# Kernel optimization log

Measured on AMD Instinct MI355X. Metric: run time of the kernel, lower is better.

## Reference

```python
import jax, jax.numpy as jnp
import numpy as np

T, B, I, H, E = 32, 128, 64, 128, 4
N_TRAP = 100  # trapezoid intervals -> 101 sample points


def setup_inputs() -> dict:
    key = jax.random.key(0)
    ks = jax.random.split(key, 14)
    s_cell = 1.0 / np.sqrt(I + H)
    s_wh = 1.0 / np.sqrt((I + H) * E)

    def u(k, shape, s):
        return jax.random.uniform(k, shape, jnp.float32, -s, s)

    return {
        "x_time": jax.random.normal(ks[0], (T, B, I), jnp.float32),
        "dt_time": jax.random.uniform(ks[1], (T, B), jnp.float32, 0.01, 1.0),
        "Wh_w": u(ks[2], ((I + H) * E, H * E), s_wh),
        "Wh_b": u(ks[3], (H * E,), s_wh),
        "Wi_w": u(ks[4], (E, I + H, H), s_cell),
        "Wi_b": u(ks[5], (E, H), s_cell),
        "Wf_w": u(ks[6], (E, I + H, H), s_cell),
        "Wf_b": u(ks[7], (E, H), s_cell),
        "Wd_w": u(ks[8], (E, I + H, H), s_cell),
        "Wd_b": u(ks[9], (E, H), s_cell),
        "Wg_w": u(ks[10], (E, I + H, H), s_cell),
        "Wg_b": u(ks[11], (E, H), s_cell),
        "Wo_w": u(ks[12], (E, I + H, H), s_cell),
        "Wo_b": u(ks[13], (E, H), s_cell),
        "alpha": jnp.ones((E, H), jnp.float32) / H,
    }


def reference(x_time, dt_time, Wh_w, Wh_b, Wi_w, Wi_b, Wf_w, Wf_b,
              Wd_w, Wd_b, Wg_w, Wg_b, Wo_w, Wo_b, alpha):
    t_total, batch, in_dim = x_time.shape
    e_types, hid = alpha.shape
    ts_unit = jnp.linspace(0.0, 1.0, N_TRAP + 1, dtype=x_time.dtype)  # [101]

    def step(carry, inp):
        h, c = carry            # each [E,B,H]
        x, dt = inp             # [B,I], [B]
        # hidden_sum = Wh(cat_m([x, h_m]))
        cat = jnp.concatenate(
            [jnp.concatenate([x, h[m]], axis=-1) for m in range(e_types)], axis=-1)  # [B,(I+H)*E]
        hs = (cat @ Wh_w + Wh_b).reshape(batch, e_types, hid).transpose(1, 0, 2)     # [E,B,H]
        iv = jnp.concatenate(
            [jnp.broadcast_to(x[None], (e_types, batch, in_dim)), hs], axis=-1)       # [E,B,I+H]

        def gate(W, b):
            return jnp.einsum('ebd,edh->ebh', iv, W) + b[:, None, :]

        i_g = jax.nn.sigmoid(gate(Wi_w, Wi_b))
        f_g = jax.nn.sigmoid(gate(Wf_w, Wf_b))
        g = f_g * c + i_g * jnp.tanh(gate(Wg_w, Wg_b))   # curr_g
        delta = jnp.exp(gate(Wd_w, Wd_b))                 # curr_delta
        o = jax.nn.sigmoid(gate(Wo_w, Wo_b))              # curr_o
        diff = c - g                                      # prev_c - curr_g

        c_new = g + diff * jnp.exp(-delta * dt[None, :, None])  # c_t at dt
        h_new = o * jnp.tanh(c_new)
        lam = jnp.einsum('eh,ebh->eb', alpha, h_new)             # intensity at dt

        # trapezoidal integration of intensity over [0, dt], 100 intervals
        ts = dt[:, None] * ts_unit                                # [B,101]
        cv = g[:, :, None, :] + diff[:, :, None, :] * jnp.exp(
            -delta[:, :, None, :] * ts[None, :, :, None])         # [E,B,101,H]
        fv = jnp.einsum('eh,ebth->ebt', alpha, o[:, :, None, :] * jnp.tanh(cv))  # [E,B,101]
        integ = (dt[None, :] / N_TRAP) * (
            jnp.sum(fv, axis=-1) - 0.5 * (fv[..., 0] + fv[..., -1]))  # [E,B]

        return (h_new, c_new), (lam.T, integ.T)  # outputs [B,E]

    h0 = jnp.zeros((e_types, batch, hid), x_time.dtype)
    c0 = jnp.zeros_like(h0)
    _, (lambdas, lambda_integrals) = jax.lax.scan(step, (h0, c0), (x_time, dt_time))
    return lambdas, lambda_integrals  # each [T,B,E]
```

## Files before the change

### kernel.cpp

```cpp
#include <hip/hip_runtime.h>

#define OFF_WALL   0
#define OFF_BIAS   196608
#define OFF_WHHH   199680
#define OFF_WGH    330752
#define OFF_XG     494592
#define OFF_HBUF   21466112

typedef _Float16 half2_t __attribute__((ext_vector_type(2)));

__device__ __forceinline__ float fast_sig(float x) {
    return __fdividef(1.f, 1.f + __expf(-x));
}
__device__ __forceinline__ float sig_e(float y) {
    return __builtin_amdgcn_rcpf(__expf(y) + 1.f);
}
__device__ __forceinline__ unsigned pack2h(float a, float b) {
    _Float16 ha = (_Float16)a, hb = (_Float16)b;
    unsigned short ua = __builtin_bit_cast(unsigned short, ha);
    unsigned short ub = __builtin_bit_cast(unsigned short, hb);
    return ((unsigned)ub << 16) | ua;
}
__device__ __forceinline__ float dot2(unsigned w, unsigned h, float acc) {
    return __builtin_amdgcn_fdot2(__builtin_bit_cast(half2_t, w),
                                  __builtin_bit_cast(half2_t, h), acc, false);
}

__global__ __launch_bounds__(256) void k0_pack(
    const float* __restrict__ Wh_w, const float* __restrict__ Wh_b,
    const float* __restrict__ Wi_w, const float* __restrict__ Wi_b,
    const float* __restrict__ Wf_w, const float* __restrict__ Wf_b,
    const float* __restrict__ Wd_w, const float* __restrict__ Wd_b,
    const float* __restrict__ Wg_w, const float* __restrict__ Wg_b,
    const float* __restrict__ Wo_w, const float* __restrict__ Wo_b,
    float* __restrict__ ws)
{
    const float* gw[5] = {Wi_w, Wf_w, Wd_w, Wg_w, Wo_w};
    const float* gb[5] = {Wi_b, Wf_b, Wd_b, Wg_b, Wo_b};
    int idx = blockIdx.x * 256 + threadIdx.x;
    if (idx < 196608) {
        int r = idx / 3072, col = idx - r * 3072;
        float v;
        if (col < 512) {
            v = Wh_w[r * 512 + col] + Wh_w[(192 + r) * 512 + col]
              + Wh_w[(384 + r) * 512 + col] + Wh_w[(576 + r) * 512 + col];
        } else {
            int q = col - 512;
            int e = q / 640;
            int rem = q - e * 640;
            int g = rem >> 7, h = rem & 127;
            v = gw[g][(e * 192 + r) * 128 + h];
        }
        ws[OFF_WALL + idx] = v;
    } else if (idx < 327680) {
        int i = idx - 196608;
        int q    = i & 3;
        int lane = (i >> 2) & 127;
        int i4   = (i >> 9) & 15;
        int kq   = (i >> 13) & 3;
        int e    = i >> 15;
        int kp = i4 * 4 + q;
        int k0 = kq * 128 + 2 * kp;
        int r0 = (k0 >> 7) * 192 + 64 + (k0 & 127);
        float w0 = Wh_w[r0 * 512 + e * 128 + lane];
        float w1 = Wh_w[(r0 + 1) * 512 + e * 128 + lane];
        reinterpret_cast<unsigned*>(ws + OFF_WHHH)[i] = pack2h(w0, w1);
    } else if (idx < 491520) {
        int i = idx - 327680;
        int lane = i & 127;
        int gg = (i >> 7) % 5;
        int rest = (i >> 7) / 5;
        int ii = rest & 15;
        int kq = (rest >> 4) & 3;
        int e  = rest >> 6;
        int k0 = kq * 32 + 2 * ii, k1 = k0 + 1;
        float w0 = gw[gg][(e * 192 + 64 + k0) * 128 + lane];
        float w1 = gw[gg][(e * 192 + 64 + k1) * 128 + lane];
        reinterpret_cast<unsigned*>(ws + OFF_WGH)[i] = pack2h(w0, w1);
    }
    if (idx < 3072) {
        float v;
        if (idx < 512) v = Wh_b[idx];
        else {
            int q = idx - 512;
            int e = q / 640;
            int rem = q - e * 640;
            int g = rem >> 7, h = rem & 127;
            v = gb[g][e * 128 + h];
        }
        ws[OFF_BIAS + idx] = v;
    }
    if (idx < 262144) {
        reinterpret_cast<unsigned*>(ws + OFF_HBUF)[idx] = 0xFFFFFFFFu;
    }
}

__global__ __launch_bounds__(256) void k1_xproj(
    const float* __restrict__ x, const float* wsr, float* XG)
{
    __shared__ __align__(16) float XT[64 * 68];
    const float* W_all = wsr + OFF_WALL;
    const float* bias  = wsr + OFF_BIAS;
    int bid = blockIdx.x;
    int ct = bid % 48, rt = bid / 48;
    int r0 = rt * 64, c0 = ct * 64;
    for (int p = threadIdx.x; p < 4096; p += 256) {
        int i = p >> 6, k = p & 63;
        XT[k * 68 + i] = x[(r0 + i) * 64 + k];
    }
    __syncthreads();
    int col = c0 + (threadIdx.x & 63);
    int iq = threadIdx.x >> 6;
    float acc[16];
    #pragma unroll
    for (int r = 0; r < 16; r++) acc[r] = 0.f;
    const float* wp = W_all + col;
    #pragma unroll 4
    for (int k = 0; k < 64; k++) {
        float w = wp[k * 3072];
        const float4* xt4 = reinterpret_cast<const float4*>(&XT[k * 68 + iq * 16]);
        #pragma unroll
        for (int r4 = 0; r4 < 4; r4++) {
            float4 xv = xt4[r4];
            acc[r4 * 4 + 0] = fmaf(xv.x, w, acc[r4 * 4 + 0]);
            acc[r4 * 4 + 1] = fmaf(xv.y, w, acc[r4 * 4 + 1]);
            acc[r4 * 4 + 2] = fmaf(xv.z, w, acc[r4 * 4 + 2]);
            acc[r4 * 4 + 3] = fmaf(xv.w, w, acc[r4 * 4 + 3]);
        }
    }
    float bv = bias[col];
    #pragma unroll
    for (int r = 0; r < 16; r++) {
        int row = r0 + iq * 16 + r;
        XG[row * 3072 + col] = acc[r] + bv;
    }
}

__global__ __launch_bounds__(512, 1) void k2_recur(
    const uint4* __restrict__ WhhH4,
    const unsigned* __restrict__ WgH,
    const float* __restrict__ XG,
    const float* __restrict__ dt_time,
    const float* __restrict__ alpha,
    unsigned* __restrict__ hbuf,
    float* __restrict__ lam_out,
    float* __restrict__ integ_out)
{
    __shared__ __align__(16) uint4 waL[8192];
    __shared__ __align__(16) unsigned hsP[2][64];
    __shared__ __align__(16) unsigned hOut[128];
    __shared__ float pA[4][2][128];
    __shared__ float pB[4][2][5][128];
    __shared__ __align__(16) float4 cellSt[256];
    __shared__ float red[4];
    __shared__ float red2[8];
    const int tid = threadIdx.x;
    const int bid = blockIdx.x;
    const int e   = (bid >> 3) & 3;
    const int grp = (bid & 7) | ((bid >> 5) << 3);
    const int b0  = grp * 2;
    const int kq  = tid >> 7;
    const int lane = tid & 127;
    const int l64 = tid & 63;
    const int s = (tid >> 7) & 1, l = lane;

    {
        const uint4* src = WhhH4 + (size_t)e * 8192;
        #pragma unroll
        for (int n = 0; n < 16; ++n) waL[tid + 512 * n] = src[tid + 512 * n];
    }
    unsigned wg[5][16];
    #pragma unroll
    for (int i = 0; i < 16; i++) {
        #pragma unroll
        for (int g = 0; g < 5; g++)
            wg[g][i] = WgH[(((e * 4 + kq) * 16 + i) * 5 + g) * 128 + lane];
    }
    const float av = alpha[e * 128 + lane];
    float cst = 0.f;
    __syncthreads();

    for (int t = 0; t < 32; ++t) {
        const int row0 = t * 128 + b0;
        float xg0 = 0.f, xgg0 = 0.f, xgg1 = 0.f, xgg2 = 0.f, xgg3 = 0.f, xgg4 = 0.f;
        if (tid < 256) {
            const float* base = XG + (size_t)(row0 + s) * 3072;
            xg0 = base[e * 128 + l];
            const float* gp = base + 512 + e * 640 + l;
            xgg0 = gp[0]; xgg1 = gp[128]; xgg2 = gp[256]; xgg3 = gp[384]; xgg4 = gp[512];
        }
        if (t > 0) {
            uint2 hu;
            if (kq == e) {
                hu.x = hOut[l64];
                hu.y = hOut[64 + l64];
            } else {
                const unsigned long long* ap =
                    reinterpret_cast<const unsigned long long*>(
                        hbuf + ((size_t)((t & 1) * 64 + grp) * 4 + e) * 512)
                    + (kq * 64 + l64);
                unsigned long long v = __hip_atomic_load(ap, __ATOMIC_RELAXED,
                                                         __HIP_MEMORY_SCOPE_AGENT);
                while (v == ~0ull) {
                    __builtin_amdgcn_s_sleep(1);
                    v = __hip_atomic_load(ap, __ATOMIC_RELAXED,
                                          __HIP_MEMORY_SCOPE_AGENT);
                }
                hu.x = (unsigned)v;
                hu.y = (unsigned)(v >> 32);
            }
            float a0 = 0.f, a1 = 0.f;
            #pragma unroll
            for (int i4 = 0; i4 < 16; ++i4) {
                uint4 w = waL[(kq * 16 + i4) * 128 + lane];
                unsigned h0, h1;
                h0 = __builtin_amdgcn_readlane(hu.x, i4 * 4 + 0);
                h1 = __builtin_amdgcn_readlane(hu.y, i4 * 4 + 0);
                a0 = dot2(w.x, h0, a0); a1 = dot2(w.x, h1, a1);
                h0 = __builtin_amdgcn_readlane(hu.x, i4 * 4 + 1);
                h1 = __builtin_amdgcn_readlane(hu.y, i4 * 4 + 1);
                a0 = dot2(w.y, h0, a0); a1 = dot2(w.y, h1, a1);
                h0 = __builtin_amdgcn_readlane(hu.x, i4 * 4 + 2);
                h1 = __builtin_amdgcn_readlane(hu.y, i4 * 4 + 2);
                a0 = dot2(w.z, h0, a0); a1 = dot2(w.z, h1, a1);
                h0 = __builtin_amdgcn_readlane(hu.x, i4 * 4 + 3);
                h1 = __builtin_amdgcn_readlane(hu.y, i4 * 4 + 3);
                a0 = dot2(w.w, h0, a0); a1 = dot2(w.w, h1, a1);
            }
            pA[kq][0][lane] = a0;
            pA[kq][1][lane] = a1;
        }
        __syncthreads();
        if (t > 0 && kq != e && lane < 64) {
            unsigned long long* ap =
                reinterpret_cast<unsigned long long*>(
                    hbuf + ((size_t)((t & 1) * 64 + grp) * 4 + e) * 512)
                + (kq * 64 + l64);
            __hip_atomic_store(ap, ~0ull, __ATOMIC_RELAXED, __HIP_MEMORY_SCOPE_AGENT);
        }
        if (tid < 256) {
            float hs = xg0;
            if (t > 0) hs += pA[0][s][l] + pA[1][s][l] + pA[2][s][l] + pA[3][s][l];
            float hi = __shfl_down(hs, 1, 64);
            if ((l & 1) == 0) hsP[s][l >> 1] = pack2h(hs, hi);
        }
        __syncthreads();
        float b0a = 0.f, b1a = 0.f, b2a = 0.f, b3a = 0.f, b4a = 0.f;
        float b0b = 0.f, b1b = 0.f, b2b = 0.f, b3b = 0.f, b4b = 0.f;
        {
            unsigned hv = hsP[(l64 >> 4) & 1][kq * 16 + (l64 & 15)];
            #pragma unroll
            for (int i = 0; i < 16; ++i) {
                unsigned h0 = __builtin_amdgcn_readlane(hv, i);
                unsigned h1 = __builtin_amdgcn_readlane(hv, 16 + i);
                b0a = dot2(wg[0][i], h0, b0a); b0b = dot2(wg[0][i], h1, b0b);
                b1a = dot2(wg[1][i], h0, b1a); b1b = dot2(wg[1][i], h1, b1b);
                b2a = dot2(wg[2][i], h0, b2a); b2b = dot2(wg[2][i], h1, b2b);
                b3a = dot2(wg[3][i], h0, b3a); b3b = dot2(wg[3][i], h1, b3b);
                b4a = dot2(wg[4][i], h0, b4a); b4b = dot2(wg[4][i], h1, b4b);
            }
        }
        pB[kq][0][0][lane] = b0a; pB[kq][0][1][lane] = b1a; pB[kq][0][2][lane] = b2a;
        pB[kq][0][3][lane] = b3a; pB[kq][0][4][lane] = b4a;
        pB[kq][1][0][lane] = b0b; pB[kq][1][1][lane] = b1b; pB[kq][1][2][lane] = b2b;
        pB[kq][1][3][lane] = b3b; pB[kq][1][4][lane] = b4b;
        __syncthreads();
        if (tid < 256) {
            float ai = pB[0][s][0][l] + pB[1][s][0][l] + pB[2][s][0][l] + pB[3][s][0][l] + xgg0;
            float af = pB[0][s][1][l] + pB[1][s][1][l] + pB[2][s][1][l] + pB[3][s][1][l] + xgg1;
            float ad = pB[0][s][2][l] + pB[1][s][2][l] + pB[2][s][2][l] + pB[3][s][2][l] + xgg2;
            float ag = pB[0][s][3][l] + pB[1][s][3][l] + pB[2][s][3][l] + pB[3][s][3][l] + xgg3;
            float ao = pB[0][s][4][l] + pB[1][s][4][l] + pB[2][s][4][l] + pB[3][s][4][l] + xgg4;
            float ig = fast_sig(ai);
            float fg = fast_sig(af);
            float dl = __expf(ad);
            float gt = tanhf(ag);
            float og = fast_sig(ao);
            float gc = fmaf(fg, cst, ig * gt);
            float df = cst - gc;
            float dtv = dt_time[row0 + s];
            cst = fmaf(df, __expf(-dl * dtv), gc);
            float hn = og * tanhf(cst);
            float4 stv;
            stv.x = 2.f * gc; stv.y = 2.f * df; stv.z = dl * dtv; stv.w = av * og;
            cellSt[tid] = stv;
            float hi = __shfl_down(hn, 1, 64);
            if ((l & 1) == 0) hOut[s * 64 + (l >> 1)] = pack2h(hn, hi);
            float lm = av * hn;
            #pragma unroll
            for (int off = 32; off > 0; off >>= 1) lm += __shfl_down(lm, off, 64);
            if ((tid & 63) == 0) red[tid >> 6] = lm;
        }
        __syncthreads();
        if (tid == 0) {
            lam_out[(row0 + 0) * 4 + e] = red[0] + red[1];
            lam_out[(row0 + 1) * 4 + e] = red[2] + red[3];
        }
        if (tid < 192) {
            int cpy = tid >> 6;
            cpy += (cpy >= e) ? 1 : 0;
            int qp = tid & 63;
            unsigned long long v =
                ((unsigned long long)hOut[64 + qp] << 32) | (unsigned long long)hOut[qp];
            unsigned long long* dst =
                reinterpret_cast<unsigned long long*>(
                    hbuf + ((size_t)(((t + 1) & 1) * 64 + grp) * 4 + cpy) * 512)
                + (e * 64 + qp);
            __hip_atomic_store(dst, v, __ATOMIC_RELAXED, __HIP_MEMORY_SCOPE_AGENT);
        }
        {
            const int x = tid & 255;
            float4 stv = cellSt[x];
            float g2 = stv.x, d2 = stv.y, q = stv.z, ao = stv.w;
            float r  = __expf(-0.01f * q);
            float r2 = r * r, r4 = r2 * r2;
            float T;
            if (tid < 256) {
                float E1 = r, E2 = r2, E3 = r2 * r, E4 = r4;
                float s1 = 0.f, s2 = 0.f, s3 = 0.f, s4 = 0.f;
                #pragma unroll
                for (int k = 0; k < 12; ++k) {
                    s1 += sig_e(fmaf(d2, E1, g2)); E1 *= r4;
                    s2 += sig_e(fmaf(d2, E2, g2)); E2 *= r4;
                    s3 += sig_e(fmaf(d2, E3, g2)); E3 *= r4;
                    s4 += sig_e(fmaf(d2, E4, g2)); E4 *= r4;
                }
                float sg0 = sig_e(g2 + d2);
                T = 48.5f - 2.f * ((s1 + s2) + (s3 + s4)) - sg0;
            } else {
                float E49 = __expf(-0.49f * q);
                float E1 = E49, E2 = E49 * r, E3 = E49 * r2, E4 = E49 * r2 * r;
                float s1 = 0.f, s2 = 0.f, s3 = 0.f, s4 = 0.f;
                #pragma unroll
                for (int k = 0; k < 13; ++k) {
                    s1 += sig_e(fmaf(d2, E1, g2)); E1 *= r4;
                    s2 += sig_e(fmaf(d2, E2, g2)); E2 *= r4;
                    s3 += sig_e(fmaf(d2, E3, g2)); E3 *= r4;
                    s4 += sig_e(fmaf(d2, E4, g2)); E4 *= r4;
                }
                float e100 = __expf(-q);
                float sg100 = sig_e(fmaf(d2, e100, g2));
                T = 51.5f - 2.f * ((s1 + s2) + (s3 + s4)) + sg100;
            }
            float v = ao * T;
            #pragma unroll
            for (int off = 32; off > 0; off >>= 1) v += __shfl_down(v, off, 64);
            if ((tid & 63) == 0) red2[tid >> 6] = v;
        }
        __syncthreads();
        if (tid < 2) {
            float dtv = dt_time[row0 + tid];
            float v = (tid == 0) ? (red2[0] + red2[1] + red2[4] + red2[5])
                                 : (red2[2] + red2[3] + red2[6] + red2[7]);
            integ_out[(row0 + tid) * 4 + e] = v * (dtv * 0.01f);
        }
    }
}

extern "C" void kernel_launch(void* const* d_in, const int* in_sizes, int n_in,
                              void* d_out, int out_size, void* d_ws, size_t ws_size,
                              hipStream_t stream)
{
    const float* x_time  = (const float*)d_in[0];
    const float* dt_time = (const float*)d_in[1];
    const float* Wh_w = (const float*)d_in[2];
    const float* Wh_b = (const float*)d_in[3];
    const float* Wi_w = (const float*)d_in[4];
    const float* Wi_b = (const float*)d_in[5];
    const float* Wf_w = (const float*)d_in[6];
    const float* Wf_b = (const float*)d_in[7];
    const float* Wd_w = (const float*)d_in[8];
    const float* Wd_b = (const float*)d_in[9];
    const float* Wg_w = (const float*)d_in[10];
    const float* Wg_b = (const float*)d_in[11];
    const float* Wo_w = (const float*)d_in[12];
    const float* Wo_b = (const float*)d_in[13];
    const float* alpha = (const float*)d_in[14];

    float* ws = (float*)d_ws;
    float* XG   = ws + OFF_XG;
    unsigned* hbuf = (unsigned*)(ws + OFF_HBUF);
    float* lam_out   = (float*)d_out;
    float* integ_out = lam_out + 32 * 128 * 4;

    k0_pack<<<3072, 256, 0, stream>>>(Wh_w, Wh_b, Wi_w, Wi_b, Wf_w, Wf_b,
                                      Wd_w, Wd_b, Wg_w, Wg_b, Wo_w, Wo_b, ws);
    k1_xproj<<<3072, 256, 0, stream>>>(x_time, ws, XG);
    k2_recur<<<256, 512, 0, stream>>>(
        (const uint4*)(ws + OFF_WHHH), (const unsigned*)(ws + OFF_WGH),
        XG, dt_time, alpha, hbuf, lam_out, integ_out);
}
```

Baseline: 212.3 us.

## Defer trapezoid integral evaluation into next step's recurrent matvec loop

The sigmoid-sum integral for step t is no longer computed at the end of step t. Its state is carried in registers and the work is interleaved into step t+1's hidden-state dot-product loop, which spends its time waiting on cross-block h exchange. The last step is finished in an epilogue after the loop. This takes the transcendental work off the serial critical path, at the cost of more live registers and an extra reduction and store per step.

```diff
diff --git a/kernel.cpp b/kernel.cpp
--- a/kernel.cpp
+++ b/kernel.cpp
@@ -178,6 +178,9 @@
     }
     const float av = alpha[e * 128 + lane];
     float cst = 0.f;
+    float tD = 0.f, tG = 0.f, tAo = 0.f, tR4 = 1.f, tTb = 0.f;
+    float tE1 = 0.f, tE2 = 0.f, tE3 = 0.f, tE4 = 0.f;
+    float tS1 = 0.f, tS2 = 0.f, tS3 = 0.f, tS4 = 0.f;
     __syncthreads();
 
     for (int t = 0; t < 32; ++t) {
@@ -226,9 +229,28 @@
                 h0 = __builtin_amdgcn_readlane(hu.x, i4 * 4 + 3);
                 h1 = __builtin_amdgcn_readlane(hu.y, i4 * 4 + 3);
                 a0 = dot2(w.w, h0, a0); a1 = dot2(w.w, h1, a1);
+                if (i4 < 12) {
+                    tS1 += sig_e(fmaf(tD, tE1, tG)); tE1 *= tR4;
+                    tS2 += sig_e(fmaf(tD, tE2, tG)); tE2 *= tR4;
+                    tS3 += sig_e(fmaf(tD, tE3, tG)); tE3 *= tR4;
+                    tS4 += sig_e(fmaf(tD, tE4, tG)); tE4 *= tR4;
+                }
+            }
+            if (tid >= 256) {
+                tS1 += sig_e(fmaf(tD, tE1, tG));
+                tS2 += sig_e(fmaf(tD, tE2, tG));
+                tS3 += sig_e(fmaf(tD, tE3, tG));
+                tS4 += sig_e(fmaf(tD, tE4, tG));
             }
             pA[kq][0][lane] = a0;
             pA[kq][1][lane] = a1;
+            {
+                float Tv = tTb - 2.f * ((tS1 + tS2) + (tS3 + tS4));
+                float v = tAo * Tv;
+                #pragma unroll
+                for (int off = 32; off > 0; off >>= 1) v += __shfl_down(v, off, 64);
+                if ((tid & 63) == 0) red2[tid >> 6] = v;
+            }
         }
         __syncthreads();
         if (t > 0 && kq != e && lane < 64) {
@@ -237,6 +259,13 @@
                     hbuf + ((size_t)((t & 1) * 64 + grp) * 4 + e) * 512)
                 + (kq * 64 + l64);
             __hip_atomic_store(ap, ~0ull, __ATOMIC_RELAXED, __HIP_MEMORY_SCOPE_AGENT);
+        }
+        if (t > 0 && tid < 2) {
+            int rowp = row0 - 128 + tid;
+            float dtv = dt_time[rowp];
+            float v = (tid == 0) ? (red2[0] + red2[1] + red2[4] + red2[5])
+                                 : (red2[2] + red2[3] + red2[6] + red2[7]);
+            integ_out[rowp * 4 + e] = v * (dtv * 0.01f);
         }
         if (tid < 256) {
             float hs = xg0;
@@ -311,48 +340,50 @@
         {
             const int x = tid & 255;
             float4 stv = cellSt[x];
-            float g2 = stv.x, d2 = stv.y, q = stv.z, ao = stv.w;
-            float r  = __expf(-0.01f * q);
-            float r2 = r * r, r4 = r2 * r2;
-            float T;
+            float g2 = stv.x, d2 = stv.y, q = stv.z;
+            tAo = stv.w;
+            tD = d2; tG = g2;
+            float r = __expf(-0.01f * q);
+            float r2 = r * r;
+            tR4 = r2 * r2;
+            tS1 = 0.f; tS2 = 0.f; tS3 = 0.f; tS4 = 0.f;
             if (tid < 256) {
-                float E1 = r, E2 = r2, E3 = r2 * r, E4 = r4;
-                float s1 = 0.f, s2 = 0.f, s3 = 0.f, s4 = 0.f;
-                #pragma unroll
-                for (int k = 0; k < 12; ++k) {
-                    s1 += sig_e(fmaf(d2, E1, g2)); E1 *= r4;
-                    s2 += sig_e(fmaf(d2, E2, g2)); E2 *= r4;
-                    s3 += sig_e(fmaf(d2, E3, g2)); E3 *= r4;
-                    s4 += sig_e(fmaf(d2, E4, g2)); E4 *= r4;
-                }
-                float sg0 = sig_e(g2 + d2);
-                T = 48.5f - 2.f * ((s1 + s2) + (s3 + s4)) - sg0;
+                tE1 = r; tE2 = r2; tE3 = r2 * r; tE4 = tR4;
+                tTb = 48.5f - sig_e(g2 + d2);
             } else {
                 float E49 = __expf(-0.49f * q);
-                float E1 = E49, E2 = E49 * r, E3 = E49 * r2, E4 = E49 * r2 * r;
-                float s1 = 0.f, s2 = 0.f, s3 = 0.f, s4 = 0.f;
-                #pragma unroll
-                for (int k = 0; k < 13; ++k) {
-                    s1 += sig_e(fmaf(d2, E1, g2)); E1 *= r4;
-                    s2 += sig_e(fmaf(d2, E2, g2)); E2 *= r4;
-                    s3 += sig_e(fmaf(d2, E3, g2)); E3 *= r4;
-                    s4 += sig_e(fmaf(d2, E4, g2)); E4 *= r4;
-                }
+                tE1 = E49; tE2 = E49 * r; tE3 = E49 * r2; tE4 = E49 * r2 * r;
                 float e100 = __expf(-q);
-                float sg100 = sig_e(fmaf(d2, e100, g2));
-                T = 51.5f - 2.f * ((s1 + s2) + (s3 + s4)) + sg100;
-            }
-            float v = ao * T;
-            #pragma unroll
-            for (int off = 32; off > 0; off >>= 1) v += __shfl_down(v, off, 64);
-            if ((tid & 63) == 0) red2[tid >> 6] = v;
-        }
+                tTb = 51.5f + sig_e(fmaf(d2, e100, g2));
+            }
+        }
+    }
+    {
+        #pragma unroll
+        for (int it = 0; it < 12; ++it) {
+            tS1 += sig_e(fmaf(tD, tE1, tG)); tE1 *= tR4;
+            tS2 += sig_e(fmaf(tD, tE2, tG)); tE2 *= tR4;
+            tS3 += sig_e(fmaf(tD, tE3, tG)); tE3 *= tR4;
+            tS4 += sig_e(fmaf(tD, tE4, tG)); tE4 *= tR4;
+        }
+        if (tid >= 256) {
+            tS1 += sig_e(fmaf(tD, tE1, tG));
+            tS2 += sig_e(fmaf(tD, tE2, tG));
+            tS3 += sig_e(fmaf(tD, tE3, tG));
+            tS4 += sig_e(fmaf(tD, tE4, tG));
+        }
+        float Tv = tTb - 2.f * ((tS1 + tS2) + (tS3 + tS4));
+        float v = tAo * Tv;
+        #pragma unroll
+        for (int off = 32; off > 0; off >>= 1) v += __shfl_down(v, off, 64);
+        if ((tid & 63) == 0) red2[tid >> 6] = v;
         __syncthreads();
         if (tid < 2) {
-            float dtv = dt_time[row0 + tid];
-            float v = (tid == 0) ? (red2[0] + red2[1] + red2[4] + red2[5])
-                                 : (red2[2] + red2[3] + red2[6] + red2[7]);
-            integ_out[(row0 + tid) * 4 + e] = v * (dtv * 0.01f);
+            int rowp = 31 * 128 + b0 + tid;
+            float dtv = dt_time[rowp];
+            float vv = (tid == 0) ? (red2[0] + red2[1] + red2[4] + red2[5])
+                                  : (red2[2] + red2[3] + red2[6] + red2[7]);
+            integ_out[rowp * 4 + e] = vv * (dtv * 0.01f);
         }
     }
 }
```

Result: slower. 235.0 us (+10.7%).

## Offload trapezoid integral to separate consumer blocks synchronized via global flags

Applied to the files above, without the earlier changes.

Launches 256 extra blocks that compute the trapezoidal intensity integral for each timestep. The recurrence blocks publish their gate states to a global buffer and then set a per-group progress flag that these blocks poll. This takes the long sigmoid-sum loop off the serial recurrence critical path. Hidden-weight LDS staging is dropped in favour of direct global reads, with launch bounds raised to two blocks per CU. The trade-offs are added global memory traffic per step, a co-residency requirement to avoid deadlock, and flag ordering that relies only on relaxed atomics.

```diff
diff --git a/kernel.cpp b/kernel.cpp
--- a/kernel.cpp
+++ b/kernel.cpp
@@ -5,7 +5,10 @@
 #define OFF_WHHH   199680
 #define OFF_WGH    330752
 #define OFF_XG     494592
+#define OFF_GST    13077504
 #define OFF_HBUF   21466112
+#define OFF_PFLAG  21728256
+#define GST_PLANE  2097152
 
 typedef _Float16 half2_t __attribute__((ext_vector_type(2)));
 
@@ -93,6 +96,9 @@
     if (idx < 262144) {
         reinterpret_cast<unsigned*>(ws + OFF_HBUF)[idx] = 0xFFFFFFFFu;
     }
+    if (idx < 256) {
+        reinterpret_cast<int*>(ws + OFF_PFLAG)[idx] = 0;
+    }
 }
 
 __global__ __launch_bounds__(256) void k1_xproj(
@@ -136,26 +142,98 @@
     }
 }
 
-__global__ __launch_bounds__(512, 1) void k2_recur(
+__global__ __launch_bounds__(512, 2) void k2_recur(
     const uint4* __restrict__ WhhH4,
     const unsigned* __restrict__ WgH,
     const float* __restrict__ XG,
     const float* __restrict__ dt_time,
     const float* __restrict__ alpha,
+    float* __restrict__ Gst,
     unsigned* __restrict__ hbuf,
+    int* __restrict__ pflag,
     float* __restrict__ lam_out,
     float* __restrict__ integ_out)
 {
-    __shared__ __align__(16) uint4 waL[8192];
     __shared__ __align__(16) unsigned hsP[2][64];
     __shared__ __align__(16) unsigned hOut[128];
     __shared__ float pA[4][2][128];
     __shared__ float pB[4][2][5][128];
-    __shared__ __align__(16) float4 cellSt[256];
     __shared__ float red[4];
-    __shared__ float red2[8];
+    __shared__ float redI[8];
     const int tid = threadIdx.x;
     const int bid = blockIdx.x;
+
+    if (bid >= 256) {
+        const int tb = bid - 256;
+        const int e3 = (tb >> 3) & 3;
+        const int g3 = (tb & 7) | ((tb >> 5) << 3);
+        const int b03 = g3 * 2;
+        const int half = tid >> 8;
+        const int s3 = (tid >> 7) & 1;
+        const int l3 = tid & 127;
+        const float av3 = alpha[e3 * 128 + l3];
+        int* pf = pflag + g3 * 4 + e3;
+        for (int t = 0; t < 32; ++t) {
+            if (tid == 0) {
+                while (__hip_atomic_load(pf, __ATOMIC_RELAXED,
+                                         __HIP_MEMORY_SCOPE_AGENT) <= t)
+                    __builtin_amdgcn_s_sleep(2);
+            }
+            __syncthreads();
+            asm volatile("" ::: "memory");
+            const int row = t * 128 + b03 + s3;
+            const size_t go = (size_t)row * 512 + e3 * 128 + l3;
+            float gc = __hip_atomic_load(&Gst[0 * GST_PLANE + go], __ATOMIC_RELAXED, __HIP_MEMORY_SCOPE_AGENT);
+            float df = __hip_atomic_load(&Gst[1 * GST_PLANE + go], __ATOMIC_RELAXED, __HIP_MEMORY_SCOPE_AGENT);
+            float dl = __hip_atomic_load(&Gst[2 * GST_PLANE + go], __ATOMIC_RELAXED, __HIP_MEMORY_SCOPE_AGENT);
+            float og = __hip_atomic_load(&Gst[3 * GST_PLANE + go], __ATOMIC_RELAXED, __HIP_MEMORY_SCOPE_AGENT);
+            float dtv = dt_time[row];
+            float g2 = 2.f * gc, d2 = 2.f * df;
+            float q  = dl * dtv;
+            float r  = __expf(-0.01f * q);
+            float r2 = r * r, r4 = r2 * r2;
+            float T;
+            if (half == 0) {
+                float E1 = r, E2 = r2, E3 = r2 * r, E4 = r4;
+                float s1 = 0.f, s2 = 0.f, s3c = 0.f, s4 = 0.f;
+                #pragma unroll
+                for (int k = 0; k < 12; ++k) {
+                    s1 += sig_e(fmaf(d2, E1, g2)); E1 *= r4;
+                    s2 += sig_e(fmaf(d2, E2, g2)); E2 *= r4;
+                    s3c += sig_e(fmaf(d2, E3, g2)); E3 *= r4;
+                    s4 += sig_e(fmaf(d2, E4, g2)); E4 *= r4;
+                }
+                T = 48.5f - 2.f * ((s1 + s2) + (s3c + s4)) - sig_e(g2 + d2);
+            } else {
+                float E49 = __expf(-0.49f * q);
+                float E1 = E49, E2 = E49 * r, E3 = E49 * r2, E4 = E49 * r2 * r;
+                float s1 = 0.f, s2 = 0.f, s3c = 0.f, s4 = 0.f;
+                #pragma unroll
+                for (int k = 0; k < 13; ++k) {
+                    s1 += sig_e(fmaf(d2, E1, g2)); E1 *= r4;
+                    s2 += sig_e(fmaf(d2, E2, g2)); E2 *= r4;
+                    s3c += sig_e(fmaf(d2, E3, g2)); E3 *= r4;
+                    s4 += sig_e(fmaf(d2, E4, g2)); E4 *= r4;
+                }
+                float e100 = __expf(-q);
+                T = 51.5f - 2.f * ((s1 + s2) + (s3c + s4)) + sig_e(fmaf(d2, e100, g2));
+            }
+            float v = av3 * og * T;
+            #pragma unroll
+            for (int off = 32; off > 0; off >>= 1) v += __shfl_down(v, off, 64);
+            if ((tid & 63) == 0) redI[tid >> 6] = v;
+            __syncthreads();
+            if (tid < 2) {
+                int row2 = t * 128 + b03 + tid;
+                float dtv2 = dt_time[row2];
+                float vv = (tid == 0) ? (redI[0] + redI[1] + redI[4] + redI[5])
+                                      : (redI[2] + redI[3] + redI[6] + redI[7]);
+                integ_out[row2 * 4 + e3] = vv * (dtv2 * 0.01f);
+            }
+        }
+        return;
+    }
+
     const int e   = (bid >> 3) & 3;
     const int grp = (bid & 7) | ((bid >> 5) << 3);
     const int b0  = grp * 2;
@@ -163,12 +241,7 @@
     const int lane = tid & 127;
     const int l64 = tid & 63;
     const int s = (tid >> 7) & 1, l = lane;
-
-    {
-        const uint4* src = WhhH4 + (size_t)e * 8192;
-        #pragma unroll
-        for (int n = 0; n < 16; ++n) waL[tid + 512 * n] = src[tid + 512 * n];
-    }
+    const uint4* wap = WhhH4 + (size_t)e * 8192 + (size_t)(kq * 16) * 128 + lane;
     unsigned wg[5][16];
     #pragma unroll
     for (int i = 0; i < 16; i++) {
@@ -177,6 +250,7 @@
             wg[g][i] = WgH[(((e * 4 + kq) * 16 + i) * 5 + g) * 128 + lane];
     }
     const float av = alpha[e * 128 + lane];
+    int* pf2 = pflag + grp * 4 + e;
     float cst = 0.f;
     __syncthreads();
 
@@ -212,7 +286,7 @@
             float a0 = 0.f, a1 = 0.f;
             #pragma unroll
             for (int i4 = 0; i4 < 16; ++i4) {
-                uint4 w = waL[(kq * 16 + i4) * 128 + lane];
+                uint4 w = wap[i4 * 128];
                 unsigned h0, h1;
                 h0 = __builtin_amdgcn_readlane(hu.x, i4 * 4 + 0);
                 h1 = __builtin_amdgcn_readlane(hu.y, i4 * 4 + 0);
@@ -281,9 +355,11 @@
             float dtv = dt_time[row0 + s];
             cst = fmaf(df, __expf(-dl * dtv), gc);
             float hn = og * tanhf(cst);
-            float4 stv;
-            stv.x = 2.f * gc; stv.y = 2.f * df; stv.z = dl * dtv; stv.w = av * og;
-            cellSt[tid] = stv;
+            size_t go = (size_t)(row0 + s) * 512 + e * 128 + l;
+            __hip_atomic_store(&Gst[0 * GST_PLANE + go], gc, __ATOMIC_RELAXED, __HIP_MEMORY_SCOPE_AGENT);
+            __hip_atomic_store(&Gst[1 * GST_PLANE + go], df, __ATOMIC_RELAXED, __HIP_MEMORY_SCOPE_AGENT);
+            __hip_atomic_store(&Gst[2 * GST_PLANE + go], dl, __ATOMIC_RELAXED, __HIP_MEMORY_SCOPE_AGENT);
+            __hip_atomic_store(&Gst[3 * GST_PLANE + go], og, __ATOMIC_RELAXED, __HIP_MEMORY_SCOPE_AGENT);
             float hi = __shfl_down(hn, 1, 64);
             if ((l & 1) == 0) hOut[s * 64 + (l >> 1)] = pack2h(hn, hi);
             float lm = av * hn;
@@ -295,6 +371,8 @@
         if (tid == 0) {
             lam_out[(row0 + 0) * 4 + e] = red[0] + red[1];
             lam_out[(row0 + 1) * 4 + e] = red[2] + red[3];
+            __hip_atomic_store(pf2, t + 1, __ATOMIC_RELAXED,
+                               __HIP_MEMORY_SCOPE_AGENT);
         }
         if (tid < 192) {
             int cpy = tid >> 6;
@@ -307,52 +385,6 @@
                     hbuf + ((size_t)(((t + 1) & 1) * 64 + grp) * 4 + cpy) * 512)
                 + (e * 64 + qp);
             __hip_atomic_store(dst, v, __ATOMIC_RELAXED, __HIP_MEMORY_SCOPE_AGENT);
-        }
-        {
-            const int x = tid & 255;
-            float4 stv = cellSt[x];
-            float g2 = stv.x, d2 = stv.y, q = stv.z, ao = stv.w;
-            float r  = __expf(-0.01f * q);
-            float r2 = r * r, r4 = r2 * r2;
-            float T;
-            if (tid < 256) {
-                float E1 = r, E2 = r2, E3 = r2 * r, E4 = r4;
-                float s1 = 0.f, s2 = 0.f, s3 = 0.f, s4 = 0.f;
-                #pragma unroll
-                for (int k = 0; k < 12; ++k) {
-                    s1 += sig_e(fmaf(d2, E1, g2)); E1 *= r4;
-                    s2 += sig_e(fmaf(d2, E2, g2)); E2 *= r4;
-                    s3 += sig_e(fmaf(d2, E3, g2)); E3 *= r4;
-                    s4 += sig_e(fmaf(d2, E4, g2)); E4 *= r4;
-                }
-                float sg0 = sig_e(g2 + d2);
-                T = 48.5f - 2.f * ((s1 + s2) + (s3 + s4)) - sg0;
-            } else {
-                float E49 = __expf(-0.49f * q);
-                float E1 = E49, E2 = E49 * r, E3 = E49 * r2, E4 = E49 * r2 * r;
-                float s1 = 0.f, s2 = 0.f, s3 = 0.f, s4 = 0.f;
-                #pragma unroll
-                for (int k = 0; k < 13; ++k) {
-                    s1 += sig_e(fmaf(d2, E1, g2)); E1 *= r4;
-                    s2 += sig_e(fmaf(d2, E2, g2)); E2 *= r4;
-                    s3 += sig_e(fmaf(d2, E3, g2)); E3 *= r4;
-                    s4 += sig_e(fmaf(d2, E4, g2)); E4 *= r4;
-                }
-                float e100 = __expf(-q);
-                float sg100 = sig_e(fmaf(d2, e100, g2));
-                T = 51.5f - 2.f * ((s1 + s2) + (s3 + s4)) + sg100;
-            }
-            float v = ao * T;
-            #pragma unroll
-            for (int off = 32; off > 0; off >>= 1) v += __shfl_down(v, off, 64);
-            if ((tid & 63) == 0) red2[tid >> 6] = v;
-        }
-        __syncthreads();
-        if (tid < 2) {
-            float dtv = dt_time[row0 + tid];
-            float v = (tid == 0) ? (red2[0] + red2[1] + red2[4] + red2[5])
-                                 : (red2[2] + red2[3] + red2[6] + red2[7]);
-            integ_out[(row0 + tid) * 4 + e] = v * (dtv * 0.01f);
         }
     }
 }
@@ -379,14 +411,16 @@
 
     float* ws = (float*)d_ws;
     float* XG   = ws + OFF_XG;
+    float* Gst  = ws + OFF_GST;
     unsigned* hbuf = (unsigned*)(ws + OFF_HBUF);
+    int* pflag = (int*)(ws + OFF_PFLAG);
     float* lam_out   = (float*)d_out;
     float* integ_out = lam_out + 32 * 128 * 4;
 
     k0_pack<<<3072, 256, 0, stream>>>(Wh_w, Wh_b, Wi_w, Wi_b, Wf_w, Wf_b,
                                       Wd_w, Wd_b, Wg_w, Wg_b, Wo_w, Wo_b, ws);
     k1_xproj<<<3072, 256, 0, stream>>>(x_time, ws, XG);
-    k2_recur<<<256, 512, 0, stream>>>(
+    k2_recur<<<512, 512, 0, stream>>>(
         (const uint4*)(ws + OFF_WHHH), (const unsigned*)(ws + OFF_WGH),
-        XG, dt_time, alpha, hbuf, lam_out, integ_out);
-}
+        XG, dt_time, alpha, Gst, hbuf, pflag, lam_out, integ_out);
+}
```

After: 284.9 us. 34.2% more time.

## Move trapezoid integration out of recurrent kernel into separate parallel kernel

Applied to the files above, without the earlier changes.

The per-step trapezoidal integral is removed from the serial recurrence kernel. Each step now writes the cell state (g, diff, delta*dt, alpha*o) to global memory, and a new kernel with 16384 blocks computes all integrals afterwards in parallel. The hidden-state broadcast is also changed: threads publish packed halves directly with 32-bit atomic stores, dropping a post-sync copy stage, and the spin check now waits on each 32-bit half separately. This shortens the critical path of each recurrent step, at the cost of extra global traffic and one more launch. The k0_pack grid is also reduced, which may matter for correctness if that kernel was not covering all elements.

```diff
diff --git a/kernel.cpp b/kernel.cpp
--- a/kernel.cpp
+++ b/kernel.cpp
@@ -5,6 +5,7 @@
 #define OFF_WHHH   199680
 #define OFF_WGH    330752
 #define OFF_XG     494592
+#define OFF_GST    13077504
 #define OFF_HBUF   21466112
 
 typedef _Float16 half2_t __attribute__((ext_vector_type(2)));
@@ -142,18 +143,16 @@
     const float* __restrict__ XG,
     const float* __restrict__ dt_time,
     const float* __restrict__ alpha,
+    float4* __restrict__ Gst4,
     unsigned* __restrict__ hbuf,
-    float* __restrict__ lam_out,
-    float* __restrict__ integ_out)
+    float* __restrict__ lam_out)
 {
     __shared__ __align__(16) uint4 waL[8192];
     __shared__ __align__(16) unsigned hsP[2][64];
     __shared__ __align__(16) unsigned hOut[128];
     __shared__ float pA[4][2][128];
     __shared__ float pB[4][2][5][128];
-    __shared__ __align__(16) float4 cellSt[256];
     __shared__ float red[4];
-    __shared__ float red2[8];
     const int tid = threadIdx.x;
     const int bid = blockIdx.x;
     const int e   = (bid >> 3) & 3;
@@ -201,7 +200,8 @@
                     + (kq * 64 + l64);
                 unsigned long long v = __hip_atomic_load(ap, __ATOMIC_RELAXED,
                                                          __HIP_MEMORY_SCOPE_AGENT);
-                while (v == ~0ull) {
+                while ((unsigned)v == 0xFFFFFFFFu ||
+                       (unsigned)(v >> 32) == 0xFFFFFFFFu) {
                     __builtin_amdgcn_s_sleep(1);
                     v = __hip_atomic_load(ap, __ATOMIC_RELAXED,
                                           __HIP_MEMORY_SCOPE_AGENT);
@@ -283,9 +283,21 @@
             float hn = og * tanhf(cst);
             float4 stv;
             stv.x = 2.f * gc; stv.y = 2.f * df; stv.z = dl * dtv; stv.w = av * og;
-            cellSt[tid] = stv;
+            Gst4[(size_t)(row0 + s) * 512 + e * 128 + l] = stv;
             float hi = __shfl_down(hn, 1, 64);
-            if ((l & 1) == 0) hOut[s * 64 + (l >> 1)] = pack2h(hn, hi);
+            if ((l & 1) == 0) {
+                unsigned pw = pack2h(hn, hi);
+                hOut[s * 64 + (l >> 1)] = pw;
+                const int wi = (e * 64 + (l >> 1)) * 2 + s;
+                unsigned* basep = hbuf + (size_t)(((t + 1) & 1) * 64 + grp) * 4 * 512;
+                #pragma unroll
+                for (int c = 0; c < 4; ++c) {
+                    if (c != e) {
+                        __hip_atomic_store(basep + (size_t)c * 512 + wi, pw,
+                                           __ATOMIC_RELAXED, __HIP_MEMORY_SCOPE_AGENT);
+                    }
+                }
+            }
             float lm = av * hn;
             #pragma unroll
             for (int off = 32; off > 0; off >>= 1) lm += __shfl_down(lm, off, 64);
@@ -296,64 +308,59 @@
             lam_out[(row0 + 0) * 4 + e] = red[0] + red[1];
             lam_out[(row0 + 1) * 4 + e] = red[2] + red[3];
         }
-        if (tid < 192) {
-            int cpy = tid >> 6;
-            cpy += (cpy >= e) ? 1 : 0;
-            int qp = tid & 63;
-            unsigned long long v =
-                ((unsigned long long)hOut[64 + qp] << 32) | (unsigned long long)hOut[qp];
-            unsigned long long* dst =
-                reinterpret_cast<unsigned long long*>(
-                    hbuf + ((size_t)(((t + 1) & 1) * 64 + grp) * 4 + cpy) * 512)
-                + (e * 64 + qp);
-            __hip_atomic_store(dst, v, __ATOMIC_RELAXED, __HIP_MEMORY_SCOPE_AGENT);
-        }
-        {
-            const int x = tid & 255;
-            float4 stv = cellSt[x];
-            float g2 = stv.x, d2 = stv.y, q = stv.z, ao = stv.w;
-            float r  = __expf(-0.01f * q);
-            float r2 = r * r, r4 = r2 * r2;
-            float T;
-            if (tid < 256) {
-                float E1 = r, E2 = r2, E3 = r2 * r, E4 = r4;
-                float s1 = 0.f, s2 = 0.f, s3 = 0.f, s4 = 0.f;
-                #pragma unroll
-                for (int k = 0; k < 12; ++k) {
-                    s1 += sig_e(fmaf(d2, E1, g2)); E1 *= r4;
-                    s2 += sig_e(fmaf(d2, E2, g2)); E2 *= r4;
-                    s3 += sig_e(fmaf(d2, E3, g2)); E3 *= r4;
-                    s4 += sig_e(fmaf(d2, E4, g2)); E4 *= r4;
-                }
-                float sg0 = sig_e(g2 + d2);
-                T = 48.5f - 2.f * ((s1 + s2) + (s3 + s4)) - sg0;
-            } else {
-                float E49 = __expf(-0.49f * q);
-                float E1 = E49, E2 = E49 * r, E3 = E49 * r2, E4 = E49 * r2 * r;
-                float s1 = 0.f, s2 = 0.f, s3 = 0.f, s4 = 0.f;
-                #pragma unroll
-                for (int k = 0; k < 13; ++k) {
-                    s1 += sig_e(fmaf(d2, E1, g2)); E1 *= r4;
-                    s2 += sig_e(fmaf(d2, E2, g2)); E2 *= r4;
-                    s3 += sig_e(fmaf(d2, E3, g2)); E3 *= r4;
-                    s4 += sig_e(fmaf(d2, E4, g2)); E4 *= r4;
-                }
-                float e100 = __expf(-q);
-                float sg100 = sig_e(fmaf(d2, e100, g2));
-                T = 51.5f - 2.f * ((s1 + s2) + (s3 + s4)) + sg100;
-            }
-            float v = ao * T;
-            #pragma unroll
-            for (int off = 32; off > 0; off >>= 1) v += __shfl_down(v, off, 64);
-            if ((tid & 63) == 0) red2[tid >> 6] = v;
-        }
-        __syncthreads();
-        if (tid < 2) {
-            float dtv = dt_time[row0 + tid];
-            float v = (tid == 0) ? (red2[0] + red2[1] + red2[4] + red2[5])
-                                 : (red2[2] + red2[3] + red2[6] + red2[7]);
-            integ_out[(row0 + tid) * 4 + e] = v * (dtv * 0.01f);
-        }
+    }
+}
+
+__global__ __launch_bounds__(256) void k3_trap(
+    const float4* __restrict__ Gst4, const float* __restrict__ dt_time,
+    float* __restrict__ integ_out)
+{
+    __shared__ float red[4];
+    const int bidx = blockIdx.x;
+    const int row = bidx >> 2;
+    const int e   = bidx & 3;
+    const int tid = threadIdx.x;
+    const int l   = tid & 127;
+    const int half = tid >> 7;
+    const float dtv = dt_time[row];
+    float4 stv = Gst4[(size_t)row * 512 + e * 128 + l];
+    float g2 = stv.x, d2 = stv.y, q = stv.z, ao = stv.w;
+    float r  = __expf(-0.01f * q);
+    float r2 = r * r, r4 = r2 * r2;
+    float T;
+    if (half == 0) {
+        float E1 = r, E2 = r2, E3 = r2 * r, E4 = r4;
+        float s1 = 0.f, s2 = 0.f, s3 = 0.f, s4 = 0.f;
+        #pragma unroll
+        for (int k = 0; k < 12; ++k) {
+            s1 += sig_e(fmaf(d2, E1, g2)); E1 *= r4;
+            s2 += sig_e(fmaf(d2, E2, g2)); E2 *= r4;
+            s3 += sig_e(fmaf(d2, E3, g2)); E3 *= r4;
+            s4 += sig_e(fmaf(d2, E4, g2)); E4 *= r4;
+        }
+        T = 48.5f - 2.f * ((s1 + s2) + (s3 + s4)) - sig_e(g2 + d2);
+    } else {
+        float E49 = __expf(-0.49f * q);
+        float E1 = E49, E2 = E49 * r, E3 = E49 * r2, E4 = E49 * r2 * r;
+        float s1 = 0.f, s2 = 0.f, s3 = 0.f, s4 = 0.f;
+        #pragma unroll
+        for (int k = 0; k < 13; ++k) {
+            s1 += sig_e(fmaf(d2, E1, g2)); E1 *= r4;
+            s2 += sig_e(fmaf(d2, E2, g2)); E2 *= r4;
+            s3 += sig_e(fmaf(d2, E3, g2)); E3 *= r4;
+            s4 += sig_e(fmaf(d2, E4, g2)); E4 *= r4;
+        }
+        float e100 = __expf(-q);
+        T = 51.5f - 2.f * ((s1 + s2) + (s3 + s4)) + sig_e(fmaf(d2, e100, g2));
+    }
+    float v = ao * T;
+    #pragma unroll
+    for (int off = 32; off > 0; off >>= 1) v += __shfl_down(v, off, 64);
+    if ((tid & 63) == 0) red[tid >> 6] = v;
+    __syncthreads();
+    if (tid == 0) {
+        float vv = (red[0] + red[1]) + (red[2] + red[3]);
+        integ_out[row * 4 + e] = vv * (dtv * 0.01f);
     }
 }
 
@@ -379,14 +386,16 @@
 
     float* ws = (float*)d_ws;
     float* XG   = ws + OFF_XG;
+    float4* Gst4 = (float4*)(ws + OFF_GST);
     unsigned* hbuf = (unsigned*)(ws + OFF_HBUF);
     float* lam_out   = (float*)d_out;
     float* integ_out = lam_out + 32 * 128 * 4;
 
-    k0_pack<<<3072, 256, 0, stream>>>(Wh_w, Wh_b, Wi_w, Wi_b, Wf_w, Wf_b,
+    k0_pack<<<1920, 256, 0, stream>>>(Wh_w, Wh_b, Wi_w, Wi_b, Wf_w, Wf_b,
                                       Wd_w, Wd_b, Wg_w, Wg_b, Wo_w, Wo_b, ws);
     k1_xproj<<<3072, 256, 0, stream>>>(x_time, ws, XG);
     k2_recur<<<256, 512, 0, stream>>>(
         (const uint4*)(ws + OFF_WHHH), (const unsigned*)(ws + OFF_WGH),
-        XG, dt_time, alpha, hbuf, lam_out, integ_out);
-}
+        XG, dt_time, alpha, Gst4, hbuf, lam_out);
+    k3_trap<<<16384, 256, 0, stream>>>(Gst4, dt_time, integ_out);
+}
```

Result: faster. 205.0 us (-3.4%).
